# Kernel tuning notes

Measured on AMD Instinct MI355X. Metric: run time of the kernel, lower is better.

## Reference

```python
import jax, jax.numpy as jnp
import numpy as np

V = 50257   # vocab_size
D = 128     # embed_dim
B = 1024    # batch of center words
C = 10      # context window size


def setup_inputs() -> dict:
    key = jax.random.key(0)
    ks = jax.random.split(key, 12)
    s = 0.05  # small init scale for linear weights
    return {
        "center_id": jax.random.randint(ks[0], (B,), 0, V),
        "context_ids": jax.random.randint(ks[1], (B, C), 0, V),
        "epsilon": jax.random.normal(ks[2], (D,), dtype=jnp.float32),
        # embedding tables init uniform(-1, 1) as in the torch module
        "emb": jax.random.uniform(ks[3], (V, D), minval=-1.0, maxval=1.0, dtype=jnp.float32),
        "prior_means": jax.random.uniform(ks[4], (V, D), minval=-1.0, maxval=1.0, dtype=jnp.float32),
        "prior_vars": jax.random.uniform(ks[5], (V, D), minval=-1.0, maxval=1.0, dtype=jnp.float32),
        "W_enc": jax.random.normal(ks[6], (2 * D, 2 * D), dtype=jnp.float32) * s,
        "b_enc": jnp.zeros((2 * D,), dtype=jnp.float32),
        "W_mean": jax.random.normal(ks[7], (2 * D, D), dtype=jnp.float32) * s,
        "b_mean": jnp.zeros((D,), dtype=jnp.float32),
        "W_var": jax.random.normal(ks[8], (2 * D, D), dtype=jnp.float32) * s,
        "b_var": jnp.zeros((D,), dtype=jnp.float32),
        "W_vocab": jax.random.normal(ks[9], (D, V), dtype=jnp.float32) * s,
        "b_vocab": jnp.zeros((V,), dtype=jnp.float32),
    }


def reference(center_id, context_ids, epsilon, emb, prior_means, prior_vars,
              W_enc, b_enc, W_mean, b_mean, W_var, b_var, W_vocab, b_vocab):
    ce = emb[center_id]                       # [B, D]
    cx = emb[context_ids]                     # [B, C, D]
    enc_in = jnp.concatenate(
        [jnp.broadcast_to(ce[:, None, :], cx.shape), cx], axis=-1)  # [B, C, 2D]
    h = jax.nn.relu(enc_in @ W_enc + b_enc).sum(axis=1)  # [B, 2D]
    mean = h @ W_mean + b_mean                           # [B, D]
    var = jax.nn.softplus(h @ W_var + b_var)             # [B, D] (diag cov s0)
    z = mean + jnp.exp(var / 2.0) * epsilon              # single shared epsilon [D]
    logits = z @ W_vocab + b_vocab                        # [B, V]
    logp = jax.nn.log_softmax(logits, axis=1)             # log(categorical)

    pm = prior_means[center_id]                           # m1 [B, D]
    pv = jax.nn.softplus(prior_vars[center_id])           # diag cov s1 [B, D]
    diff = pm - mean
    # closed-form diagonal Gaussian KL, identical math to the
    # trace/inverse/det formulation over diagflat matrices in the source
    kl = 0.5 * jnp.sum(var / pv + diff * diff / pv - 1.0
                       + jnp.log(pv) - jnp.log(var), axis=1)  # [B]

    # reconstruction: sum_k log categorical[i, context_ids[i, k]]
    rec = jnp.take_along_axis(logp, context_ids, axis=1).sum(axis=1)  # [B]

    return jnp.mean(rec - kl)
```

## Files before the change

### kernel.cpp

```cpp
#include <hip/hip_runtime.h>
#include <math.h>

#define VV 50257
#define VPAD 50304
#define DD 128
#define BB 1024
#define CC 10

typedef short bf16x8 __attribute__((ext_vector_type(8)));
typedef float f32x4 __attribute__((ext_vector_type(4)));

__device__ inline float bf2f(unsigned short u) {
    return __uint_as_float(((unsigned)u) << 16);
}
__device__ inline unsigned short f2bf(float f) {
    unsigned u = __float_as_uint(f);
    unsigned r = ((u >> 16) & 1) + 0x7FFF;
    return (unsigned short)((u + r) >> 16);
}


__global__ __launch_bounds__(256) void k_prep0(
    const float* __restrict__ W_enc, unsigned short* __restrict__ WeP)
{
    __shared__ float tl[256][17];
    const int jg = blockIdx.x, tid = threadIdx.x;
#pragma unroll
    for (int i = 0; i < 16; ++i) {
        int idx = i * 256 + tid;
        int k = idx >> 4, j = idx & 15;
        tl[k][j] = W_enc[(size_t)k * 256 + jg * 16 + j];
    }
    __syncthreads();
#pragma unroll
    for (int i = 0; i < 2; ++i) {
        int c = i * 256 + tid;
        int l15 = c & 15, q = (c >> 4) & 3, kI = c >> 6;
        bf16x8 o;
#pragma unroll
        for (int e = 0; e < 8; ++e)
            o[e] = (short)f2bf(tl[kI * 32 + q * 8 + e][l15]);
        *(bf16x8*)(WeP + (((size_t)jg * 8 + kI) * 64 + q * 16 + l15) * 8) = o;
    }
}

#define AS_STRIDE 520
__global__ __launch_bounds__(256) void k_main(
    const int* __restrict__ center_id, const int* __restrict__ context_ids,
    const float* __restrict__ emb, const unsigned short* __restrict__ WeP,
    const float* __restrict__ b_enc, const float* __restrict__ Wv,
    const float* __restrict__ W_mean, const float* __restrict__ W_var,
    unsigned short* __restrict__ WvP, unsigned short* __restrict__ Wmv,
    unsigned short* __restrict__ enc_relu)
{
    __shared__ __align__(16) unsigned char smraw[50688];
    const int bid = blockIdx.x, tid = threadIdx.x;

    if (bid >= 1106) {
        const int b4 = bid - 1106;
#pragma unroll
        for (int i = 0; i < 32; ++i) {
            int idx = b4 * 8192 + i * 256 + tid;
            unsigned short m = f2bf(W_mean[idx]);
            unsigned short v = f2bf(W_var[idx]);
            *(ushort2*)(Wmv + (size_t)idx * 2) = make_ushort2(m, v);
        }
        return;
    }

    if (bid >= 320) {
        float (*tile)[65] = (float (*)[65])smraw;
        const int s = bid - 320;
        const int v0 = s * 64;
#pragma unroll
        for (int i = 0; i < 32; ++i) {
            int idx = tid + i * 256;
            int k = idx >> 6, j = idx & 63;
            int v = v0 + j;
            tile[k][j] = (v < VV) ? Wv[(size_t)k * VV + v] : 0.f;
        }
        __syncthreads();
#pragma unroll
        for (int i = 0; i < 4; ++i) {
            int c = i * 256 + tid;
            int l15 = c & 15, q = (c >> 4) & 3, kI = (c >> 6) & 3, g = c >> 8;
            bf16x8 o;
#pragma unroll
            for (int e = 0; e < 8; ++e)
                o[e] = (short)f2bf(tile[kI * 32 + q * 8 + e][g * 16 + l15]);
            size_t vg = (size_t)s * 4 + g;
            *(bf16x8*)(WvP + ((vg * 4 + kI) * 64 + q * 16 + l15) * 8) = o;
        }
        return;
    }

    unsigned short* As = (unsigned short*)smraw;
    unsigned short (*Cs)[136] = (unsigned short (*)[136])(smraw + 33280);

    const int lane = tid & 63;
    const int wid  = tid >> 6;
    const int wm   = wid & 1;
    const int wn   = wid >> 1;
    const int quad = lane >> 4;
    const int l15  = lane & 15;

    const int bt = bid & 15;
    const int c  = (bid >> 4) % 10;
    const int zt = bid / 160;
    const int b0 = bt * 64;
    const int n0 = zt * 128;

    const int rlane = tid >> 4;
    const int c8    = tid & 15;
    const int kIc   = c8 >> 2, qc = c8 & 3;
#pragma unroll
    for (int p = 0; p < 4; ++p) {
        int r = p * 16 + rlane;
        int rid_ce = center_id[b0 + r];
        int rid_cx = context_ids[(b0 + r) * CC + c];
        const float* s0 = emb + (size_t)rid_ce * 128 + c8 * 8;
        const float* s1 = emb + (size_t)rid_cx * 128 + c8 * 8;
        float4 a0 = *(const float4*)s0, a1 = *(const float4*)(s0 + 4);
        float4 b0v = *(const float4*)s1, b1v = *(const float4*)(s1 + 4);
        bf16x8 oa, ob;
        oa[0] = (short)f2bf(a0.x); oa[1] = (short)f2bf(a0.y);
        oa[2] = (short)f2bf(a0.z); oa[3] = (short)f2bf(a0.w);
        oa[4] = (short)f2bf(a1.x); oa[5] = (short)f2bf(a1.y);
        oa[6] = (short)f2bf(a1.z); oa[7] = (short)f2bf(a1.w);
        ob[0] = (short)f2bf(b0v.x); ob[1] = (short)f2bf(b0v.y);
        ob[2] = (short)f2bf(b0v.z); ob[3] = (short)f2bf(b0v.w);
        ob[4] = (short)f2bf(b1v.x); ob[5] = (short)f2bf(b1v.y);
        ob[6] = (short)f2bf(b1v.z); ob[7] = (short)f2bf(b1v.w);
        *(bf16x8*)(As + (size_t)(p * 8 + kIc) * AS_STRIDE + (qc * 16 + rlane) * 8) = oa;
        *(bf16x8*)(As + (size_t)(p * 8 + kIc + 4) * AS_STRIDE + (qc * 16 + rlane) * 8) = ob;
    }
    __syncthreads();

    float benc[4];
#pragma unroll
    for (int nt = 0; nt < 4; ++nt)
        benc[nt] = b_enc[n0 + wn * 64 + nt * 16 + l15];

    f32x4 acc[2][4];
#pragma unroll
    for (int mt = 0; mt < 2; ++mt)
#pragma unroll
        for (int nt = 0; nt < 4; ++nt) acc[mt][nt] = (f32x4){0.f, 0.f, 0.f, 0.f};

#pragma unroll
    for (int kI = 0; kI < 8; ++kI) {
        bf16x8 a[2], b[4];
#pragma unroll
        for (int mt = 0; mt < 2; ++mt)
            a[mt] = *(const bf16x8*)(As + (size_t)((wm * 2 + mt) * 8 + kI) * AS_STRIDE + lane * 8);
#pragma unroll
        for (int nt = 0; nt < 4; ++nt) {
            size_t jg = (size_t)zt * 8 + wn * 4 + nt;
            b[nt] = *(const bf16x8*)(WeP + ((jg * 8 + kI) * 64 + lane) * 8);
        }
#pragma unroll
        for (int mt = 0; mt < 2; ++mt)
#pragma unroll
            for (int nt = 0; nt < 4; ++nt)
                acc[mt][nt] = __builtin_amdgcn_mfma_f32_16x16x32_bf16(
                    a[mt], b[nt], acc[mt][nt], 0, 0, 0);
    }

#pragma unroll
    for (int mt = 0; mt < 2; ++mt)
#pragma unroll
        for (int nt = 0; nt < 4; ++nt) {
            int col = wn * 64 + nt * 16 + l15;
#pragma unroll
            for (int reg = 0; reg < 4; ++reg) {
                int row = wm * 32 + mt * 16 + quad * 4 + reg;
                Cs[row][col] = f2bf(fmaxf(acc[mt][nt][reg] + benc[nt], 0.f));
            }
        }
    __syncthreads();
#pragma unroll
    for (int i = 0; i < 4; ++i) {
        int ch = i * 256 + tid;
        int row = ch >> 4, cc = ch & 15;
        bf16x8 v = *(const bf16x8*)&Cs[row][cc * 8];
        *(bf16x8*)(enc_relu + ((size_t)(b0 + row) * CC + c) * 256 + n0 + cc * 8) = v;
    }
}

__global__ __launch_bounds__(512) void k_latent(
    const unsigned short* __restrict__ enc_relu, const unsigned short* __restrict__ Wmv,
    const float* __restrict__ b_mean, const float* __restrict__ b_var,
    const float* __restrict__ epsilon,
    const int* __restrict__ center_id, const int* __restrict__ context_ids,
    const unsigned short* __restrict__ WvP, const float* __restrict__ bv,
    const float* __restrict__ prior_means, const float* __restrict__ prior_vars,
    unsigned short* __restrict__ z_pack, float* __restrict__ kl,
    float* __restrict__ ctxsum, float* __restrict__ out)
{
    __shared__ __align__(16) float hs[4][256];
    __shared__ float mpart[3][4][128], vpart[3][4][128];
    __shared__ float zsh[4][128];
    __shared__ float red[4][2];
    __shared__ float credw[4][2];
    const int tid = threadIdx.x;
    const int b0 = blockIdx.x * 4;

    if (blockIdx.x == 0 && tid == 0) out[0] = 0.f;

    {
        const int col = tid & 255;
        const int rr  = tid >> 8;
#pragma unroll
        for (int r2 = 0; r2 < 2; ++r2) {
            int row = rr * 2 + r2;
            float s = 0.f;
#pragma unroll
            for (int c = 0; c < CC; ++c)
                s += bf2f(enc_relu[((size_t)(b0 + row) * CC + c) * 256 + col]);
            hs[row][col] = s;
        }
    }
    __syncthreads();

    const int d    = tid & 127;
    const int part = tid >> 7;
    const int kbase = part * 64;
    float m[4], vr[4];
#pragma unroll
    for (int r = 0; r < 4; ++r) {
        m[r]  = part ? 0.f : b_mean[d];
        vr[r] = part ? 0.f : b_var[d];
    }
    for (int k0 = 0; k0 < 64; k0 += 4) {
        float4 h4[4];
#pragma unroll
        for (int r = 0; r < 4; ++r)
            h4[r] = *(const float4*)&hs[r][kbase + k0];
#pragma unroll
        for (int kk = 0; kk < 4; ++kk) {
            ushort2 u = *(const ushort2*)(Wmv + ((size_t)(kbase + k0 + kk) * 128 + d) * 2);
            float wm_ = bf2f(u.x), wv_ = bf2f(u.y);
#pragma unroll
            for (int r = 0; r < 4; ++r) {
                float hk = ((const float*)&h4[r])[kk];
                m[r]  += hk * wm_;
                vr[r] += hk * wv_;
            }
        }
    }
    if (part) {
#pragma unroll
        for (int r = 0; r < 4; ++r) {
            mpart[part - 1][r][d] = m[r];
            vpart[part - 1][r][d] = vr[r];
        }
    }
    __syncthreads();

    if (tid < 128) {
        const int wid = tid >> 6;
        const int kIz = d >> 5, qz = (d >> 3) & 3, ez = d & 7;
        const int bg = b0 >> 4;
#pragma unroll
        for (int r = 0; r < 4; ++r) {
            float mm = m[r]  + mpart[0][r][d] + mpart[1][r][d] + mpart[2][r][d];
            float vv = vr[r] + vpart[0][r][d] + vpart[1][r][d] + vpart[2][r][d];

            float var = (vv > 20.f) ? vv : log1pf(__expf(vv));
            float zd = mm + __expf(0.5f * var) * epsilon[d];
            unsigned short zu = f2bf(zd);
            const int bb = b0 + r;
            const int l15b = bb & 15;
            z_pack[(((size_t)(bg * 4 + kIz)) * 64 + qz * 16 + l15b) * 8 + ez] = zu;
            zsh[r][d] = bf2f(zu);

            int cid = center_id[bb];
            float pm  = prior_means[(size_t)cid * 128 + d];
            float pvr = prior_vars[(size_t)cid * 128 + d];
            float pv  = (pvr > 20.f) ? pvr : log1pf(__expf(pvr));
            float diff = pm - mm;
            float t = var / pv + diff * diff / pv - 1.f + logf(pv) - logf(var);
#pragma unroll
            for (int off = 32; off; off >>= 1) t += __shfl_xor(t, off, 64);
            if ((tid & 63) == 0) red[r][wid] = t;
        }
    }
    __syncthreads();

    {
        const int w     = tid >> 6;
        const int row   = w & 3;
        const int phalf = w >> 2;
        const int lane  = tid & 63;
        const float z1 = zsh[row][lane];
        const float z2 = zsh[row][lane + 64];
        const int kI1 = lane >> 5, q1 = (lane >> 3) & 3, e1 = lane & 7;
        const int d2  = lane + 64;
        const int kI2 = d2 >> 5,  q2 = (d2 >> 3) & 3,  e2 = d2 & 7;
        float cacc = 0.f;
#pragma unroll
        for (int pp = 0; pp < 5; ++pp) {
            int p = phalf * 5 + pp;
            int cid = context_ids[(b0 + row) * CC + p];
            int vg = cid >> 4, l15v = cid & 15;
            float w1 = bf2f(WvP[(((size_t)(vg * 4 + kI1)) * 64 + q1 * 16 + l15v) * 8 + e1]);
            float w2 = bf2f(WvP[(((size_t)(vg * 4 + kI2)) * 64 + q2 * 16 + l15v) * 8 + e2]);
            float cs = z1 * w1 + z2 * w2;
#pragma unroll
            for (int off = 32; off; off >>= 1) cs += __shfl_xor(cs, off, 64);
            cacc += cs + bv[cid];
        }
        if (lane == 0) credw[row][phalf] = cacc;
    }
    __syncthreads();
    if (tid < 4) {
        kl[b0 + tid]     = 0.5f * (red[tid][0] + red[tid][1]);
        ctxsum[b0 + tid] = credw[tid][0] + credw[tid][1];
    }
}

__global__ __launch_bounds__(256) void k_lse(
    const unsigned short* __restrict__ z_pack, const unsigned short* __restrict__ WvP,
    const float* __restrict__ bv, float* __restrict__ partial)
{
    __shared__ float pl[2][128][20];
    const int x = blockIdx.x + 8 * blockIdx.y;
    if (x >= 393) return;
    const int mg = blockIdx.z;

    const int tid  = threadIdx.x;
    const int lane = tid & 63;
    const int wid  = tid >> 6;
    const int wm   = wid & 1;
    const int wn   = wid >> 1;
    const int quad = lane >> 4;
    const int l15  = lane & 15;
    const int n0   = x * 128;

    bf16x8 bfr[4][4];
#pragma unroll
    for (int nt = 0; nt < 4; ++nt) {
        size_t vg = (size_t)x * 8 + wn * 4 + nt;
#pragma unroll
        for (int kI = 0; kI < 4; ++kI)
            bfr[nt][kI] = *(const bf16x8*)(WvP + ((vg * 4 + kI) * 64 + lane) * 8);
    }

    float bvf[4];
#pragma unroll
    for (int nt = 0; nt < 4; ++nt) {
        int n = n0 + wn * 64 + nt * 16 + l15;
        bvf[nt] = (n < VV) ? bv[n] : -__builtin_huge_valf();
    }

#pragma unroll
    for (int mi = 0; mi < 2; ++mi) {
        const int mi_g = mg * 2 + mi;

        f32x4 acc[4][4];
#pragma unroll
        for (int mt = 0; mt < 4; ++mt)
#pragma unroll
            for (int nt = 0; nt < 4; ++nt) acc[mt][nt] = (f32x4){0.f, 0.f, 0.f, 0.f};

#pragma unroll
        for (int kI = 0; kI < 4; ++kI) {
            bf16x8 afr[4];
#pragma unroll
            for (int mt = 0; mt < 4; ++mt) {
                size_t bg = (size_t)mi_g * 8 + wm * 4 + mt;
                afr[mt] = *(const bf16x8*)(z_pack + ((bg * 4 + kI) * 64 + lane) * 8);
            }
#pragma unroll
            for (int mt = 0; mt < 4; ++mt)
#pragma unroll
                for (int nt = 0; nt < 4; ++nt)
                    acc[mt][nt] = __builtin_amdgcn_mfma_f32_16x16x32_bf16(
                        afr[mt], bfr[nt][kI], acc[mt][nt], 0, 0, 0);
        }

#pragma unroll
        for (int mt = 0; mt < 4; ++mt)
#pragma unroll
            for (int reg = 0; reg < 4; ++reg) {
                float s = 0.f;
#pragma unroll
                for (int nt = 0; nt < 4; ++nt)
                    s += __expf(acc[mt][nt][reg] + bvf[nt]);
                pl[wn][wm * 64 + mt * 16 + quad * 4 + reg][l15] = s;
            }
        __syncthreads();
        if (tid < 128) {
            const float* p0 = &pl[0][tid][0];
            const float* p1 = &pl[1][tid][0];
            float4 a0 = *(const float4*)(p0);
            float4 a1 = *(const float4*)(p0 + 4);
            float4 a2 = *(const float4*)(p0 + 8);
            float4 a3 = *(const float4*)(p0 + 12);
            float4 b0 = *(const float4*)(p1);
            float4 b1 = *(const float4*)(p1 + 4);
            float4 b2 = *(const float4*)(p1 + 8);
            float4 b3 = *(const float4*)(p1 + 12);
            float tot = (a0.x + a0.y + a0.z + a0.w) + (a1.x + a1.y + a1.z + a1.w)
                      + (a2.x + a2.y + a2.z + a2.w) + (a3.x + a3.y + a3.z + a3.w)
                      + (b0.x + b0.y + b0.z + b0.w) + (b1.x + b1.y + b1.z + b1.w)
                      + (b2.x + b2.y + b2.z + b2.w) + (b3.x + b3.y + b3.z + b3.w);
            partial[(size_t)x * 1024 + mi_g * 128 + tid] = tot;
        }
        __syncthreads();
    }
}

__global__ __launch_bounds__(256) void k_reduce(
    const float* __restrict__ partial, const float* __restrict__ ctxsum,
    const float* __restrict__ kl, float* __restrict__ out)
{
    __shared__ float bred[4];
    const int tid = threadIdx.x;
    const int row = blockIdx.x * 16 + (tid >> 4);
    const int part = tid & 15;

    float s = 0.f;
    for (int vb = part; vb < 393; vb += 16)
        s += partial[(size_t)vb * 1024 + row];
    s += __shfl_xor(s, 1, 64);
    s += __shfl_xor(s, 2, 64);
    s += __shfl_xor(s, 4, 64);
    s += __shfl_xor(s, 8, 64);

    float v = 0.f;
    if (part == 0)
        v = ctxsum[row] - 10.f * logf(s) - kl[row];
    v += __shfl_xor(v, 16, 64);
    v += __shfl_xor(v, 32, 64);
    if ((tid & 63) == 0) bred[tid >> 6] = v;
    __syncthreads();
    if (tid == 0)
        atomicAdd(out, (bred[0] + bred[1] + bred[2] + bred[3]) * (1.f / 1024.f));
}

extern "C" void kernel_launch(void* const* d_in, const int* in_sizes, int n_in,
                              void* d_out, int out_size, void* d_ws, size_t ws_size,
                              hipStream_t stream)
{
    const int*   center_id   = (const int*)d_in[0];
    const int*   context_ids = (const int*)d_in[1];
    const float* epsilon     = (const float*)d_in[2];
    const float* emb         = (const float*)d_in[3];
    const float* prior_means = (const float*)d_in[4];
    const float* prior_vars  = (const float*)d_in[5];
    const float* W_enc       = (const float*)d_in[6];
    const float* b_enc       = (const float*)d_in[7];
    const float* W_mean      = (const float*)d_in[8];
    const float* b_mean      = (const float*)d_in[9];
    const float* W_var       = (const float*)d_in[10];
    const float* b_var       = (const float*)d_in[11];
    const float* W_vocab     = (const float*)d_in[12];
    const float* b_vocab     = (const float*)d_in[13];

    float* out = (float*)d_out;
    char*  ws  = (char*)d_ws;

    size_t off = 0;
    unsigned short* WvP      = (unsigned short*)(ws + off); off += 12877824;
    unsigned short* WeP      = (unsigned short*)(ws + off); off += 131072;
    unsigned short* Wmv      = (unsigned short*)(ws + off); off += 131072;
    unsigned short* z_pack   = (unsigned short*)(ws + off); off += 262144;
    unsigned short* enc_relu = (unsigned short*)(ws + off); off += 5242880;
    float*          kl       = (float*)(ws + off);          off += 4096;
    float*          ctxsum   = (float*)(ws + off);          off += 4096;
    float*          partial  = (float*)(ws + off);          off += 1609728;

    k_prep0<<<16, 256, 0, stream>>>(W_enc, WeP);
    k_main<<<1110, 256, 0, stream>>>(center_id, context_ids, emb, WeP, b_enc,
                                     W_vocab, W_mean, W_var, WvP, Wmv, enc_relu);
    k_latent<<<256, 512, 0, stream>>>(enc_relu, Wmv, b_mean, b_var, epsilon,
                                      center_id, context_ids, WvP, b_vocab,
                                      prior_means, prior_vars, z_pack, kl,
                                      ctxsum, out);
    k_lse<<<dim3(8, 50, 4), 256, 0, stream>>>(z_pack, WvP, b_vocab, partial);
    k_reduce<<<64, 256, 0, stream>>>(partial, ctxsum, kl, out);
}
```

Before: 201.1 us.

## Fuse context-sum into encoder kernel and fold final reduction into LSE kernel

The encoder kernel now loops over all 10 context positions per block. It computes the center-embedding half of the GEMM once, keeps the context-side weights in registers, and accumulates the ReLU sum into fp32 h directly. This replaces writing a 5 MB bf16 enc_relu buffer and re-reading it in the latent kernel, and cuts the encoder grid from 320 to 32 blocks. The LSE kernel processes twice as many batch tiles per block. A ticket counter lets the last 64 blocks spin-wait and perform the final reduction, removing the separate reduce kernel launch. The risks are reduced parallelism in the encoder stage and the spin-wait relying on all blocks being resident or scheduled.

Result: slower. 259.1 us (+28.8%).

```diff
diff --git a/kernel.cpp b/kernel.cpp
--- a/kernel.cpp
+++ b/kernel.cpp
@@ -21,10 +21,12 @@
 
 
 __global__ __launch_bounds__(256) void k_prep0(
-    const float* __restrict__ W_enc, unsigned short* __restrict__ WeP)
+    const float* __restrict__ W_enc, unsigned short* __restrict__ WeP,
+    unsigned int* __restrict__ counter)
 {
     __shared__ float tl[256][17];
     const int jg = blockIdx.x, tid = threadIdx.x;
+    if (jg == 0 && tid == 0) counter[0] = 0u;
 #pragma unroll
     for (int i = 0; i < 16; ++i) {
         int idx = i * 256 + tid;
@@ -51,13 +53,13 @@
     const float* __restrict__ b_enc, const float* __restrict__ Wv,
     const float* __restrict__ W_mean, const float* __restrict__ W_var,
     unsigned short* __restrict__ WvP, unsigned short* __restrict__ Wmv,
-    unsigned short* __restrict__ enc_relu)
+    float* __restrict__ h)
 {
     __shared__ __align__(16) unsigned char smraw[50688];
     const int bid = blockIdx.x, tid = threadIdx.x;
 
-    if (bid >= 1106) {
-        const int b4 = bid - 1106;
+    if (bid >= 818) {
+        const int b4 = bid - 818;
 #pragma unroll
         for (int i = 0; i < 32; ++i) {
             int idx = b4 * 8192 + i * 256 + tid;
@@ -68,9 +70,9 @@
         return;
     }
 
-    if (bid >= 320) {
+    if (bid >= 32) {
         float (*tile)[65] = (float (*)[65])smraw;
-        const int s = bid - 320;
+        const int s = bid - 32;
         const int v0 = s * 64;
 #pragma unroll
         for (int i = 0; i < 32; ++i) {
@@ -95,7 +97,6 @@
     }
 
     unsigned short* As = (unsigned short*)smraw;
-    unsigned short (*Cs)[136] = (unsigned short (*)[136])(smraw + 33280);
 
     const int lane = tid & 63;
     const int wid  = tid >> 6;
@@ -105,33 +106,38 @@
     const int l15  = lane & 15;
 
     const int bt = bid & 15;
-    const int c  = (bid >> 4) % 10;
-    const int zt = bid / 160;
+    const int zt = bid >> 4;
     const int b0 = bt * 64;
     const int n0 = zt * 128;
 
     const int rlane = tid >> 4;
     const int c8    = tid & 15;
     const int kIc   = c8 >> 2, qc = c8 & 3;
+
 #pragma unroll
     for (int p = 0; p < 4; ++p) {
         int r = p * 16 + rlane;
         int rid_ce = center_id[b0 + r];
-        int rid_cx = context_ids[(b0 + r) * CC + c];
         const float* s0 = emb + (size_t)rid_ce * 128 + c8 * 8;
-        const float* s1 = emb + (size_t)rid_cx * 128 + c8 * 8;
         float4 a0 = *(const float4*)s0, a1 = *(const float4*)(s0 + 4);
-        float4 b0v = *(const float4*)s1, b1v = *(const float4*)(s1 + 4);
-        bf16x8 oa, ob;
+        bf16x8 oa;
         oa[0] = (short)f2bf(a0.x); oa[1] = (short)f2bf(a0.y);
         oa[2] = (short)f2bf(a0.z); oa[3] = (short)f2bf(a0.w);
         oa[4] = (short)f2bf(a1.x); oa[5] = (short)f2bf(a1.y);
         oa[6] = (short)f2bf(a1.z); oa[7] = (short)f2bf(a1.w);
+        *(bf16x8*)(As + (size_t)(p * 8 + kIc) * AS_STRIDE + (qc * 16 + rlane) * 8) = oa;
+    }
+#pragma unroll
+    for (int p = 0; p < 4; ++p) {
+        int r = p * 16 + rlane;
+        int rid_cx = context_ids[(b0 + r) * CC + 0];
+        const float* s1 = emb + (size_t)rid_cx * 128 + c8 * 8;
+        float4 b0v = *(const float4*)s1, b1v = *(const float4*)(s1 + 4);
+        bf16x8 ob;
         ob[0] = (short)f2bf(b0v.x); ob[1] = (short)f2bf(b0v.y);
         ob[2] = (short)f2bf(b0v.z); ob[3] = (short)f2bf(b0v.w);
         ob[4] = (short)f2bf(b1v.x); ob[5] = (short)f2bf(b1v.y);
         ob[6] = (short)f2bf(b1v.z); ob[7] = (short)f2bf(b1v.w);
-        *(bf16x8*)(As + (size_t)(p * 8 + kIc) * AS_STRIDE + (qc * 16 + rlane) * 8) = oa;
         *(bf16x8*)(As + (size_t)(p * 8 + kIc + 4) * AS_STRIDE + (qc * 16 + rlane) * 8) = ob;
     }
     __syncthreads();
@@ -141,14 +147,22 @@
     for (int nt = 0; nt < 4; ++nt)
         benc[nt] = b_enc[n0 + wn * 64 + nt * 16 + l15];
 
-    f32x4 acc[2][4];
+    bf16x8 bbot[4][4];
+#pragma unroll
+    for (int nt = 0; nt < 4; ++nt) {
+        size_t jg = (size_t)zt * 8 + wn * 4 + nt;
+#pragma unroll
+        for (int kI = 0; kI < 4; ++kI)
+            bbot[nt][kI] = *(const bf16x8*)(WeP + ((jg * 8 + kI + 4) * 64 + lane) * 8);
+    }
+
+    f32x4 acc_ce[2][4];
 #pragma unroll
     for (int mt = 0; mt < 2; ++mt)
 #pragma unroll
-        for (int nt = 0; nt < 4; ++nt) acc[mt][nt] = (f32x4){0.f, 0.f, 0.f, 0.f};
-
-#pragma unroll
-    for (int kI = 0; kI < 8; ++kI) {
+        for (int nt = 0; nt < 4; ++nt) acc_ce[mt][nt] = (f32x4){0.f, 0.f, 0.f, 0.f};
+#pragma unroll
+    for (int kI = 0; kI < 4; ++kI) {
         bf16x8 a[2], b[4];
 #pragma unroll
         for (int mt = 0; mt < 2; ++mt)
@@ -162,10 +176,66 @@
         for (int mt = 0; mt < 2; ++mt)
 #pragma unroll
             for (int nt = 0; nt < 4; ++nt)
-                acc[mt][nt] = __builtin_amdgcn_mfma_f32_16x16x32_bf16(
-                    a[mt], b[nt], acc[mt][nt], 0, 0, 0);
-    }
-
+                acc_ce[mt][nt] = __builtin_amdgcn_mfma_f32_16x16x32_bf16(
+                    a[mt], b[nt], acc_ce[mt][nt], 0, 0, 0);
+    }
+
+    float hacc[2][4][4];
+#pragma unroll
+    for (int mt = 0; mt < 2; ++mt)
+#pragma unroll
+        for (int nt = 0; nt < 4; ++nt)
+#pragma unroll
+            for (int reg = 0; reg < 4; ++reg) hacc[mt][nt][reg] = 0.f;
+
+    for (int c = 0; c < CC; ++c) {
+        f32x4 acc[2][4];
+#pragma unroll
+        for (int mt = 0; mt < 2; ++mt)
+#pragma unroll
+            for (int nt = 0; nt < 4; ++nt) acc[mt][nt] = acc_ce[mt][nt];
+#pragma unroll
+        for (int kI = 0; kI < 4; ++kI) {
+            bf16x8 a[2];
+#pragma unroll
+            for (int mt = 0; mt < 2; ++mt)
+                a[mt] = *(const bf16x8*)(As + (size_t)((wm * 2 + mt) * 8 + kI + 4) * AS_STRIDE + lane * 8);
+#pragma unroll
+            for (int mt = 0; mt < 2; ++mt)
+#pragma unroll
+                for (int nt = 0; nt < 4; ++nt)
+                    acc[mt][nt] = __builtin_amdgcn_mfma_f32_16x16x32_bf16(
+                        a[mt], bbot[nt][kI], acc[mt][nt], 0, 0, 0);
+        }
+#pragma unroll
+        for (int mt = 0; mt < 2; ++mt)
+#pragma unroll
+            for (int nt = 0; nt < 4; ++nt)
+#pragma unroll
+                for (int reg = 0; reg < 4; ++reg)
+                    hacc[mt][nt][reg] += fmaxf(acc[mt][nt][reg] + benc[nt], 0.f);
+
+        if (c < CC - 1) {
+            __syncthreads();
+#pragma unroll
+            for (int p = 0; p < 4; ++p) {
+                int r = p * 16 + rlane;
+                int rid_cx = context_ids[(b0 + r) * CC + (c + 1)];
+                const float* s1 = emb + (size_t)rid_cx * 128 + c8 * 8;
+                float4 b0v = *(const float4*)s1, b1v = *(const float4*)(s1 + 4);
+                bf16x8 ob;
+                ob[0] = (short)f2bf(b0v.x); ob[1] = (short)f2bf(b0v.y);
+                ob[2] = (short)f2bf(b0v.z); ob[3] = (short)f2bf(b0v.w);
+                ob[4] = (short)f2bf(b1v.x); ob[5] = (short)f2bf(b1v.y);
+                ob[6] = (short)f2bf(b1v.z); ob[7] = (short)f2bf(b1v.w);
+                *(bf16x8*)(As + (size_t)(p * 8 + kIc + 4) * AS_STRIDE + (qc * 16 + rlane) * 8) = ob;
+            }
+            __syncthreads();
+        }
+    }
+
+    __syncthreads();
+    float (*Csf)[132] = (float (*)[132])smraw;
 #pragma unroll
     for (int mt = 0; mt < 2; ++mt)
 #pragma unroll
@@ -174,21 +244,20 @@
 #pragma unroll
             for (int reg = 0; reg < 4; ++reg) {
                 int row = wm * 32 + mt * 16 + quad * 4 + reg;
-                Cs[row][col] = f2bf(fmaxf(acc[mt][nt][reg] + benc[nt], 0.f));
+                Csf[row][col] = hacc[mt][nt][reg];
             }
         }
     __syncthreads();
 #pragma unroll
-    for (int i = 0; i < 4; ++i) {
-        int ch = i * 256 + tid;
-        int row = ch >> 4, cc = ch & 15;
-        bf16x8 v = *(const bf16x8*)&Cs[row][cc * 8];
-        *(bf16x8*)(enc_relu + ((size_t)(b0 + row) * CC + c) * 256 + n0 + cc * 8) = v;
+    for (int it = 0; it < 8; ++it) {
+        int ch = it * 256 + tid;
+        int row = ch >> 5, cg = ch & 31;
+        *(float4*)&h[(size_t)(b0 + row) * 256 + n0 + cg * 4] = *(const float4*)&Csf[row][cg * 4];
     }
 }
 
 __global__ __launch_bounds__(512) void k_latent(
-    const unsigned short* __restrict__ enc_relu, const unsigned short* __restrict__ Wmv,
+    const float* __restrict__ h, const unsigned short* __restrict__ Wmv,
     const float* __restrict__ b_mean, const float* __restrict__ b_var,
     const float* __restrict__ epsilon,
     const int* __restrict__ center_id, const int* __restrict__ context_ids,
@@ -213,11 +282,7 @@
 #pragma unroll
         for (int r2 = 0; r2 < 2; ++r2) {
             int row = rr * 2 + r2;
-            float s = 0.f;
-#pragma unroll
-            for (int c = 0; c < CC; ++c)
-                s += bf2f(enc_relu[((size_t)(b0 + row) * CC + c) * 256 + col]);
-            hs[row][col] = s;
+            hs[row][col] = h[(size_t)(b0 + row) * 256 + col];
         }
     }
     __syncthreads();
@@ -319,124 +384,139 @@
     }
 }
 
+#define LSE_BLOCKS 800
+#define RED_BLOCKS 64
 __global__ __launch_bounds__(256) void k_lse(
     const unsigned short* __restrict__ z_pack, const unsigned short* __restrict__ WvP,
-    const float* __restrict__ bv, float* __restrict__ partial)
+    const float* __restrict__ bv, float* __restrict__ partial,
+    const float* __restrict__ ctxsum, const float* __restrict__ kl,
+    unsigned int* __restrict__ counter, float* __restrict__ out)
 {
     __shared__ float pl[2][128][20];
+    __shared__ float bred[4];
+    __shared__ unsigned int ticket;
     const int x = blockIdx.x + 8 * blockIdx.y;
-    if (x >= 393) return;
     const int mg = blockIdx.z;
-
     const int tid  = threadIdx.x;
-    const int lane = tid & 63;
-    const int wid  = tid >> 6;
-    const int wm   = wid & 1;
-    const int wn   = wid >> 1;
-    const int quad = lane >> 4;
-    const int l15  = lane & 15;
-    const int n0   = x * 128;
-
-    bf16x8 bfr[4][4];
-#pragma unroll
-    for (int nt = 0; nt < 4; ++nt) {
-        size_t vg = (size_t)x * 8 + wn * 4 + nt;
-#pragma unroll
-        for (int kI = 0; kI < 4; ++kI)
-            bfr[nt][kI] = *(const bf16x8*)(WvP + ((vg * 4 + kI) * 64 + lane) * 8);
-    }
-
-    float bvf[4];
-#pragma unroll
-    for (int nt = 0; nt < 4; ++nt) {
-        int n = n0 + wn * 64 + nt * 16 + l15;
-        bvf[nt] = (n < VV) ? bv[n] : -__builtin_huge_valf();
-    }
-
-#pragma unroll
-    for (int mi = 0; mi < 2; ++mi) {
-        const int mi_g = mg * 2 + mi;
-
-        f32x4 acc[4][4];
-#pragma unroll
-        for (int mt = 0; mt < 4; ++mt)
-#pragma unroll
-            for (int nt = 0; nt < 4; ++nt) acc[mt][nt] = (f32x4){0.f, 0.f, 0.f, 0.f};
-
-#pragma unroll
-        for (int kI = 0; kI < 4; ++kI) {
-            bf16x8 afr[4];
-#pragma unroll
-            for (int mt = 0; mt < 4; ++mt) {
-                size_t bg = (size_t)mi_g * 8 + wm * 4 + mt;
-                afr[mt] = *(const bf16x8*)(z_pack + ((bg * 4 + kI) * 64 + lane) * 8);
+
+    if (x < 393) {
+        const int lane = tid & 63;
+        const int wid  = tid >> 6;
+        const int wm   = wid & 1;
+        const int wn   = wid >> 1;
+        const int quad = lane >> 4;
+        const int l15  = lane & 15;
+        const int n0   = x * 128;
+
+        bf16x8 bfr[4][4];
+#pragma unroll
+        for (int nt = 0; nt < 4; ++nt) {
+            size_t vg = (size_t)x * 8 + wn * 4 + nt;
+#pragma unroll
+            for (int kI = 0; kI < 4; ++kI)
+                bfr[nt][kI] = *(const bf16x8*)(WvP + ((vg * 4 + kI) * 64 + lane) * 8);
+        }
+
+        float bvf[4];
+#pragma unroll
+        for (int nt = 0; nt < 4; ++nt) {
+            int n = n0 + wn * 64 + nt * 16 + l15;
+            bvf[nt] = (n < VV) ? bv[n] : -__builtin_huge_valf();
+        }
+
+#pragma unroll
+        for (int mi = 0; mi < 4; ++mi) {
+            const int mi_g = mg * 4 + mi;
+
+            f32x4 acc[4][4];
+#pragma unroll
+            for (int mt = 0; mt < 4; ++mt)
+#pragma unroll
+                for (int nt = 0; nt < 4; ++nt) acc[mt][nt] = (f32x4){0.f, 0.f, 0.f, 0.f};
+
+#pragma unroll
+            for (int kI = 0; kI < 4; ++kI) {
+                bf16x8 afr[4];
+#pragma unroll
+                for (int mt = 0; mt < 4; ++mt) {
+                    size_t bg = (size_t)mi_g * 8 + wm * 4 + mt;
+                    afr[mt] = *(const bf16x8*)(z_pack + ((bg * 4 + kI) * 64 + lane) * 8);
+                }
+#pragma unroll
+                for (int mt = 0; mt < 4; ++mt)
+#pragma unroll
+                    for (int nt = 0; nt < 4; ++nt)
+                        acc[mt][nt] = __builtin_amdgcn_mfma_f32_16x16x32_bf16(
+                            afr[mt], bfr[nt][kI], acc[mt][nt], 0, 0, 0);
             }
+
 #pragma unroll
             for (int mt = 0; mt < 4; ++mt)
 #pragma unroll
-                for (int nt = 0; nt < 4; ++nt)
-                    acc[mt][nt] = __builtin_amdgcn_mfma_f32_16x16x32_bf16(
-                        afr[mt], bfr[nt][kI], acc[mt][nt], 0, 0, 0);
-        }
-
-#pragma unroll
-        for (int mt = 0; mt < 4; ++mt)
-#pragma unroll
-            for (int reg = 0; reg < 4; ++reg) {
-                float s = 0.f;
-#pragma unroll
-                for (int nt = 0; nt < 4; ++nt)
-                    s += __expf(acc[mt][nt][reg] + bvf[nt]);
-                pl[wn][wm * 64 + mt * 16 + quad * 4 + reg][l15] = s;
+                for (int reg = 0; reg < 4; ++reg) {
+                    float s = 0.f;
+#pragma unroll
+                    for (int nt = 0; nt < 4; ++nt)
+                        s += __expf(acc[mt][nt][reg] + bvf[nt]);
+                    pl[wn][wm * 64 + mt * 16 + quad * 4 + reg][l15] = s;
+                }
+            __syncthreads();
+            if (tid < 128) {
+                const float* p0 = &pl[0][tid][0];
+                const float* p1 = &pl[1][tid][0];
+                float4 a0 = *(const float4*)(p0);
+                float4 a1 = *(const float4*)(p0 + 4);
+                float4 a2 = *(const float4*)(p0 + 8);
+                float4 a3 = *(const float4*)(p0 + 12);
+                float4 b0 = *(const float4*)(p1);
+                float4 b1 = *(const float4*)(p1 + 4);
+                float4 b2 = *(const float4*)(p1 + 8);
+                float4 b3 = *(const float4*)(p1 + 12);
+                float tot = (a0.x + a0.y + a0.z + a0.w) + (a1.x + a1.y + a1.z + a1.w)
+                          + (a2.x + a2.y + a2.z + a2.w) + (a3.x + a3.y + a3.z + a3.w)
+                          + (b0.x + b0.y + b0.z + b0.w) + (b1.x + b1.y + b1.z + b1.w)
+                          + (b2.x + b2.y + b2.z + b2.w) + (b3.x + b3.y + b3.z + b3.w);
+                partial[(size_t)x * 1024 + mi_g * 128 + tid] = tot;
             }
-        __syncthreads();
-        if (tid < 128) {
-            const float* p0 = &pl[0][tid][0];
-            const float* p1 = &pl[1][tid][0];
-            float4 a0 = *(const float4*)(p0);
-            float4 a1 = *(const float4*)(p0 + 4);
-            float4 a2 = *(const float4*)(p0 + 8);
-            float4 a3 = *(const float4*)(p0 + 12);
-            float4 b0 = *(const float4*)(p1);
-            float4 b1 = *(const float4*)(p1 + 4);
-            float4 b2 = *(const float4*)(p1 + 8);
-            float4 b3 = *(const float4*)(p1 + 12);
-            float tot = (a0.x + a0.y + a0.z + a0.w) + (a1.x + a1.y + a1.z + a1.w)
-                      + (a2.x + a2.y + a2.z + a2.w) + (a3.x + a3.y + a3.z + a3.w)
-                      + (b0.x + b0.y + b0.z + b0.w) + (b1.x + b1.y + b1.z + b1.w)
-                      + (b2.x + b2.y + b2.z + b2.w) + (b3.x + b3.y + b3.z + b3.w);
-            partial[(size_t)x * 1024 + mi_g * 128 + tid] = tot;
-        }
-        __syncthreads();
-    }
-}
-
-__global__ __launch_bounds__(256) void k_reduce(
-    const float* __restrict__ partial, const float* __restrict__ ctxsum,
-    const float* __restrict__ kl, float* __restrict__ out)
-{
-    __shared__ float bred[4];
-    const int tid = threadIdx.x;
-    const int row = blockIdx.x * 16 + (tid >> 4);
-    const int part = tid & 15;
-
-    float s = 0.f;
-    for (int vb = part; vb < 393; vb += 16)
-        s += partial[(size_t)vb * 1024 + row];
-    s += __shfl_xor(s, 1, 64);
-    s += __shfl_xor(s, 2, 64);
-    s += __shfl_xor(s, 4, 64);
-    s += __shfl_xor(s, 8, 64);
-
-    float v = 0.f;
-    if (part == 0)
-        v = ctxsum[row] - 10.f * logf(s) - kl[row];
-    v += __shfl_xor(v, 16, 64);
-    v += __shfl_xor(v, 32, 64);
-    if ((tid & 63) == 0) bred[tid >> 6] = v;
-    __syncthreads();
-    if (tid == 0)
-        atomicAdd(out, (bred[0] + bred[1] + bred[2] + bred[3]) * (1.f / 1024.f));
+            __syncthreads();
+        }
+    }
+
+    __threadfence();
+    if (tid == 0) ticket = atomicAdd(counter, 1u);
+    __syncthreads();
+    const unsigned int old = ticket;
+    if (old >= (unsigned)(LSE_BLOCKS - RED_BLOCKS)) {
+        const int slice = (int)old - (LSE_BLOCKS - RED_BLOCKS);
+        if (slice < RED_BLOCKS) {
+            if (tid == 0) {
+                while (atomicAdd(counter, 0u) < (unsigned)LSE_BLOCKS)
+                    __builtin_amdgcn_s_sleep(2);
+            }
+            __syncthreads();
+            __threadfence();
+
+            const int row = slice * 16 + (tid >> 4);
+            const int part = tid & 15;
+            float s = 0.f;
+            for (int vb = part; vb < 393; vb += 16)
+                s += partial[(size_t)vb * 1024 + row];
+            s += __shfl_xor(s, 1, 64);
+            s += __shfl_xor(s, 2, 64);
+            s += __shfl_xor(s, 4, 64);
+            s += __shfl_xor(s, 8, 64);
+
+            float v = 0.f;
+            if (part == 0)
+                v = ctxsum[row] - 10.f * logf(s) - kl[row];
+            v += __shfl_xor(v, 16, 64);
+            v += __shfl_xor(v, 32, 64);
+            if ((tid & 63) == 0) bred[tid >> 6] = v;
+            __syncthreads();
+            if (tid == 0)
+                atomicAdd(out, (bred[0] + bred[1] + bred[2] + bred[3]) * (1.f / 1024.f));
+        }
+    }
 }
 
 extern "C" void kernel_launch(void* const* d_in, const int* in_sizes, int n_in,
@@ -466,18 +546,19 @@
     unsigned short* WeP      = (unsigned short*)(ws + off); off += 131072;
     unsigned short* Wmv      = (unsigned short*)(ws + off); off += 131072;
     unsigned short* z_pack   = (unsigned short*)(ws + off); off += 262144;
-    unsigned short* enc_relu = (unsigned short*)(ws + off); off += 5242880;
+    float*          h        = (float*)(ws + off);          off += 1048576;
     float*          kl       = (float*)(ws + off);          off += 4096;
     float*          ctxsum   = (float*)(ws + off);          off += 4096;
     float*          partial  = (float*)(ws + off);          off += 1609728;
-
-    k_prep0<<<16, 256, 0, stream>>>(W_enc, WeP);
-    k_main<<<1110, 256, 0, stream>>>(center_id, context_ids, emb, WeP, b_enc,
-                                     W_vocab, W_mean, W_var, WvP, Wmv, enc_relu);
-    k_latent<<<256, 512, 0, stream>>>(enc_relu, Wmv, b_mean, b_var, epsilon,
+    unsigned int*   counter  = (unsigned int*)(ws + off);   off += 4096;
+
+    k_prep0<<<16, 256, 0, stream>>>(W_enc, WeP, counter);
+    k_main<<<822, 256, 0, stream>>>(center_id, context_ids, emb, WeP, b_enc,
+                                    W_vocab, W_mean, W_var, WvP, Wmv, h);
+    k_latent<<<256, 512, 0, stream>>>(h, Wmv, b_mean, b_var, epsilon,
                                       center_id, context_ids, WvP, b_vocab,
                                       prior_means, prior_vars, z_pack, kl,
                                       ctxsum, out);
-    k_lse<<<dim3(8, 50, 4), 256, 0, stream>>>(z_pack, WvP, b_vocab, partial);
-    k_reduce<<<64, 256, 0, stream>>>(partial, ctxsum, kl, out);
-}
+    k_lse<<<dim3(8, 50, 2), 256, 0, stream>>>(z_pack, WvP, b_vocab, partial,
+                                              ctxsum, kl, counter, out);
+}
```
